# Kernel optimization log

Measured on AMD Instinct MI355X. Metric: run time of the kernel, lower is better.

Reference implementation:

```python
import jax, jax.numpy as jnp
import numpy as np

N_ELEC, N_NUC, D, F, E = 1024, 256, 64, 64, 131072
HH, HG = 128, 128
# labels: en (elec->nuc), ne (nuc->elec), same (elec->elec), anti (elec->elec)
SRC_N = [N_ELEC, N_NUC, N_ELEC, N_ELEC]
TGT_N = [N_NUC, N_ELEC, N_ELEC, N_ELEC]


def setup_inputs() -> dict:
    key = jax.random.key(0)
    ks = jax.random.split(key, 16)
    s_elec = jax.random.normal(ks[0], (N_ELEC, D), jnp.float32)
    v_elec = jax.random.normal(ks[1], (N_ELEC, D, 3), jnp.float32)
    s_nuc = jax.random.normal(ks[2], (N_NUC, D), jnp.float32)
    v_nuc = jax.random.normal(ks[3], (N_NUC, D, 3), jnp.float32)
    senders = jnp.stack([jax.random.randint(jax.random.fold_in(ks[4], i), (E,), 0, SRC_N[i]) for i in range(4)]).astype(jnp.int32)
    receivers = jnp.stack([jax.random.randint(jax.random.fold_in(ks[5], i), (E,), 0, TGT_N[i]) for i in range(4)]).astype(jnp.int32)
    dist = jax.random.uniform(ks[6], (4, E, F), jnp.float32)
    dirs = jax.random.normal(ks[7], (4, E, 3), jnp.float32)
    dirs = dirs / jnp.linalg.norm(dirs, axis=-1, keepdims=True)  # unit directions
    def w_init(k, shape):
        return jax.random.normal(k, shape, jnp.float32) / jnp.sqrt(jnp.float32(shape[-2]))
    return {
        's_elec': s_elec, 'v_elec': v_elec, 's_nuc': s_nuc, 'v_nuc': v_nuc,
        'dist': dist, 'dirs': dirs,
        'W_w': w_init(ks[8], (4, F, 3 * D)),
        'W_h1': w_init(ks[9], (4, D, HH)), 'W_h2': w_init(ks[10], (4, HH, 3 * D)),
        'W_g1': w_init(ks[11], (4, 2 * D, HG)), 'W_g2': w_init(ks[12], (4, HG, 3 * D)),
        'W_V': jnp.broadcast_to(jnp.eye(D, dtype=jnp.float32), (4, D, D)),
        'W_U': jnp.broadcast_to(jnp.eye(D, dtype=jnp.float32), (4, D, D)),
        'senders': senders, 'receivers': receivers,
    }


def _painn_layer(s_elec, v_elec, s_nuc, v_nuc, dist, dirs, W_w, W_h1, W_h2, W_g1, W_g2, W_V, W_U, senders, receivers):
    src_s = [s_elec, s_nuc, s_elec, s_elec]
    src_v = [v_elec, v_nuc, v_elec, v_elec]
    ds_e = jnp.zeros_like(s_elec); dv_e = jnp.zeros_like(v_elec)
    ds_n = jnp.zeros_like(s_nuc); dv_n = jnp.zeros_like(v_nuc)
    for i in range(4):
        n_tgt = TGT_N[i]
        # edge MLPs: w (1-layer, last linear) and h (2-layer silu, last linear), bias-free
        we = dist[i] @ W_w[i]                                   # [E, 3D]
        h_all = jax.nn.silu(src_s[i] @ W_h1[i]) @ W_h2[i]        # [n_src, 3D]
        hx = h_all[senders[i]]                                   # gather per edge
        phi_s, phi_vv, phi_vs = jnp.split(we * hx, 3, axis=-1)   # each [E, D]
        z_s = jax.ops.segment_sum(phi_s, receivers[i], n_tgt)    # [n_tgt, D]
        vv = phi_vv[..., None] * src_v[i][senders[i]]            # [E, D, 3]
        vs = phi_vs[..., None] * dirs[i][:, None, :]             # [E, D, 3]
        z_v = jax.ops.segment_sum(vv + vs, receivers[i], n_tgt)  # [n_tgt, D, 3]
        Vv = jnp.einsum('ndi,df->nfi', z_v, W_V[i])
        Uv = jnp.einsum('ndi,df->nfi', z_v, W_U[i])
        g_in = jnp.concatenate([z_s, (Vv ** 2).sum(axis=-1)], axis=-1)  # [n_tgt, 2D]
        gs = jax.nn.silu(g_in @ W_g1[i]) @ W_g2[i]               # [n_tgt, 3D]
        a_ss, a_vv, a_sv = jnp.split(gs, 3, axis=-1)
        upd_v = Uv * a_vv[..., None]
        upd_s = a_sv * jnp.einsum('nfi,nfi->nf', Uv, Vv) + a_ss
        if i == 0:  # 'en' -> nuclei
            ds_n = ds_n + upd_s; dv_n = dv_n + upd_v
        else:       # 'ne','same','anti' -> electrons
            ds_e = ds_e + upd_s; dv_e = dv_e + upd_v
    s_e = s_elec + ds_e
    v_e = v_elec + dv_e
    return jnp.concatenate([s_e, v_e.reshape(N_ELEC, -1)], axis=-1)


def reference(s_elec, v_elec, s_nuc, v_nuc, dist, dirs, W_w, W_h1, W_h2, W_g1, W_g2, W_V, W_U, senders, receivers):
    return _painn_layer(s_elec, v_elec, s_nuc, v_nuc, dist, dirs, W_w, W_h1, W_h2, W_g1, W_g2, W_V, W_U, senders, receivers)
```

## Files before the change

kernel.cpp:

```cpp
#include <hip/hip_runtime.h>
#include <stdint.h>

#define E_EDGES 131072
#define NELEC 1024
#define NNUC 256
#define MAXCHUNK 256
#define NBLK 16

typedef unsigned short ushort_t;
typedef __attribute__((ext_vector_type(8))) short short8;
typedef __attribute__((ext_vector_type(4))) short short4_t;
typedef __attribute__((ext_vector_type(4))) float float4_t;
typedef __attribute__((ext_vector_type(4))) int int4_t;
typedef __attribute__((ext_vector_type(2))) unsigned int uint2_t;

__device__ inline float silu_f(float x){ return x / (1.0f + expf(-x)); }

__device__ inline short f2bf_rne(float x){
    union { float f; uint32_t u; } a; a.f = x;
    return (short)((a.u + 0x7fffu + ((a.u >> 16) & 1u)) >> 16);
}
__device__ inline float bf2f(short h){
    union { uint32_t u; float f; } a; a.u = ((uint32_t)(uint16_t)h) << 16;
    return a.f;
}
__device__ inline ushort_t bfu(float x){ return (ushort_t)f2bf_rne(x); }
__device__ inline float asf_lo(uint32_t u){ union { uint32_t u; float f; } a; a.u = u << 16; return a.f; }
__device__ inline float asf_hi(uint32_t u){ union { uint32_t u; float f; } a; a.u = u & 0xFFFF0000u; return a.f; }

__global__ __launch_bounds__(256) void prep_kernel(
    const float* __restrict__ s_elec, const float* __restrict__ v_elec,
    const float* __restrict__ s_nuc,  const float* __restrict__ v_nuc,
    const float* __restrict__ W_h1, const float* __restrict__ W_h2,
    const float* __restrict__ W_w,
    const int* __restrict__ receivers,
    ushort_t* __restrict__ tabA, ushort_t* __restrict__ tabB,
    short* __restrict__ fragH, short* __restrict__ fragL,
    int* __restrict__ bh, float* __restrict__ out)
{
    int b = blockIdx.x, tid = threadIdx.x;
    __shared__ float sls[8][64];
    __shared__ float hidls[128][8];
    __shared__ int hist[1024];

    if (b < 288){
        int t, node0;
        if (b < 32){ t = 0; node0 = b*8; }
        else if (b < 160){ t = 1; node0 = (b-32)*8; }
        else { t = 2; node0 = (b-160)*8; }
        int tp = t + 1;
        const float* src = (t == 0) ? s_nuc : s_elec;
        const float* vsrc = (t == 0) ? v_nuc : v_elec;
        long baseA = (t == 0) ? 0 : (t == 1 ? 32768 : 163840);
        long baseB = (t == 0) ? 0 : (t == 1 ? 65536 : 327680);
        for (int i = tid; i < 512; i += 256){ int n = i >> 6, f = i & 63; sls[n][f] = src[(node0+n)*64 + f]; }
        __syncthreads();
        {
            int j = tid & 127, nh = tid >> 7;
            const float* w1 = W_h1 + (long)tp*64*128;
            float a0=0,a1=0,a2=0,a3=0;
            #pragma unroll 8
            for (int f = 0; f < 64; f++){
                float w = w1[f*128 + j];
                a0 += sls[nh*4+0][f]*w; a1 += sls[nh*4+1][f]*w;
                a2 += sls[nh*4+2][f]*w; a3 += sls[nh*4+3][f]*w;
            }
            float4_t hv = { silu_f(a0), silu_f(a1), silu_f(a2), silu_f(a3) };
            *(float4_t*)&hidls[j][nh*4] = hv;
        }
        __syncthreads();
        if (tid < 192){
            const float* w2 = W_h2 + (long)tp*128*192;
            float acc[8] = {0,0,0,0,0,0,0,0};
            #pragma unroll 4
            for (int h = 0; h < 128; h++){
                float w = w2[h*192 + tid];
                float4_t ha = *(float4_t*)&hidls[h][0];
                float4_t hb = *(float4_t*)&hidls[h][4];
                acc[0]+=ha[0]*w; acc[1]+=ha[1]*w; acc[2]+=ha[2]*w; acc[3]+=ha[3]*w;
                acc[4]+=hb[0]*w; acc[5]+=hb[1]*w; acc[6]+=hb[2]*w; acc[7]+=hb[3]*w;
            }
            int p = tid >> 6, d2 = tid & 63;
            if (p == 0){
                #pragma unroll
                for (int n = 0; n < 8; n++)
                    tabA[baseA + (long)((node0+n)*64 + d2)*2 + 0] = bfu(acc[n]);
            } else if (p == 2){
                #pragma unroll
                for (int n = 0; n < 8; n++)
                    tabA[baseA + (long)((node0+n)*64 + d2)*2 + 1] = bfu(acc[n]);
            } else {
                #pragma unroll
                for (int n = 0; n < 8; n++){
                    const float* vp = vsrc + (long)(node0+n)*192 + d2*3;
                    long o = baseB + (long)((node0+n)*64 + d2)*4;
                    tabB[o+0] = bfu(acc[n]*vp[0]);
                    tabB[o+1] = bfu(acc[n]*vp[1]);
                    tabB[o+2] = bfu(acc[n]*vp[2]);
                }
            }
        }
    } else if (b < 291){
        int t = b - 288, tp = t + 1;
        const float* W = W_w + (long)tp*64*192;
        for (int idx = tid; idx < 12288; idx += 256){
            int j    = idx & 7;
            int lane = (idx >> 3) & 63;
            int ks   = (idx >> 9) & 1;
            int nt   = idx >> 10;
            int k = ks*32 + ((lane >> 4) & 3)*8 + j;
            int n = nt*16 + (lane & 15);
            float v = W[k*192 + n];
            short hi = f2bf_rne(v);
            short lo = f2bf_rne(v - bf2f(hi));
            fragH[t*12288 + idx] = hi;
            fragL[t*12288 + idx] = lo;
        }
    } else if (b < 547){
        int i = (b - 291)*256 + tid;
        int n = i >> 6, c4 = i & 63;
        float4_t v;
        if (c4 < 16) v = *(const float4_t*)(s_elec + n*64 + c4*4);
        else         v = *(const float4_t*)(v_elec + n*192 + (c4-16)*4);
        *(float4_t*)(out + n*256 + c4*4) = v;
    } else {
        int hb = b - 547, t = hb >> 4, blk = hb & 15;
        for (int i = tid; i < 1024; i += 256) hist[i] = 0;
        __syncthreads();
        long base = (long)(t+1)*E_EDGES + blk*8192;
        #pragma unroll 4
        for (int it = 0; it < 32; it++){
            int r = receivers[base + it*256 + tid];
            atomicAdd(&hist[r], 1);
        }
        __syncthreads();
        for (int bin = tid; bin < 1024; bin += 256)
            bh[(t*1024 + bin)*NBLK + blk] = hist[bin];
    }
}

__global__ __launch_bounds__(1024) void scan_kernel(int* __restrict__ bh,
                                                    int* __restrict__ offs,
                                                    int* __restrict__ counts){
    __shared__ int buf[1024];
    int tid = threadIdx.x;
    int base = tid*48;
    int vals[48];
    const int4_t* p = (const int4_t*)(bh + base);
    int s = 0;
    #pragma unroll
    for (int j = 0; j < 12; j++){
        int4_t x = p[j];
        vals[j*4+0]=x[0]; vals[j*4+1]=x[1]; vals[j*4+2]=x[2]; vals[j*4+3]=x[3];
        s += x[0]+x[1]+x[2]+x[3];
    }
    buf[tid] = s;
    __syncthreads();
    int x = s;
    for (int off = 1; off < 1024; off <<= 1){
        int y = (tid >= off) ? buf[tid - off] : 0;
        __syncthreads();
        x += y; buf[tid] = x;
        __syncthreads();
    }
    int run = x - s;
    #pragma unroll
    for (int k = 0; k < 3; k++){
        int tb = tid*3 + k;
        offs[tb] = run;
        int c = 0;
        #pragma unroll
        for (int j = 0; j < 16; j++){
            int v = vals[k*16 + j];
            bh[base + k*16 + j] = run;
            run += v; c += v;
        }
        counts[tb] = c;
    }
}

__global__ __launch_bounds__(256) void scatter_kernel(const int* __restrict__ receivers,
                                                      const int* __restrict__ senders,
                                                      const int* __restrict__ bh,
                                                      int* __restrict__ sorted){
    int hb = blockIdx.x, t = hb >> 4, blk = hb & 15;
    int tid = threadIdx.x;
    __shared__ int cur[1024];
    for (int bin = tid; bin < 1024; bin += 256) cur[bin] = bh[(t*1024 + bin)*NBLK + blk];
    __syncthreads();
    long base = (long)(t+1)*E_EDGES + blk*8192;
    #pragma unroll 2
    for (int it = 0; it < 32; it++){
        int e = blk*8192 + it*256 + tid;
        int r = receivers[base + it*256 + tid];
        int snd = senders[base + it*256 + tid];
        int pos = atomicAdd(&cur[r], 1);
        sorted[pos] = e | (snd << 17);
    }
}

__global__ __launch_bounds__(256) void main_kernel(
    const float* __restrict__ dist, const float* __restrict__ dirs,
    const float* __restrict__ W_V, const float* __restrict__ W_U,
    const float* __restrict__ W_g1, const float* __restrict__ W_g2,
    const ushort_t* __restrict__ tabA, const ushort_t* __restrict__ tabB,
    const short* __restrict__ fragH, const short* __restrict__ fragL,
    const int* __restrict__ counts, const int* __restrict__ offs, const int* __restrict__ sorted,
    float* __restrict__ out)
{
    int b = blockIdx.x;
    int t = b >> 10, node = b & 1023, tp = t + 1;
    const ushort_t* ta = tabA + ((t == 0) ? 0 : (t == 1 ? 32768 : 163840));
    const ushort_t* tb = tabB + ((t == 0) ? 0 : (t == 1 ? 65536 : 327680));
    const float* dbase = dist + (long)tp*E_EDGES*64;
    const float* dirbase = dirs + (long)tp*E_EDGES*3;

    int tid = threadIdx.x;
    int w = tid >> 6, l = tid & 63;
    int q = l >> 4, c16 = l & 15;
    int d = w*16 + c16;

    __shared__ short AH[2][2][64][8];
    __shared__ short AL[2][2][64][8];
    __shared__ float dls[2][16][3];
    __shared__ int eid[MAXCHUNK];
    __shared__ int sid[MAXCHUNK];
    __shared__ float zs[64];
    __shared__ float zv[64][3];
    __shared__ float VvL[192], UvL[192];
    __shared__ float gin[128], hidl[128], aL[192], vdotL[64];

    short8 bhf[3][2], blf[3][2];
    #pragma unroll
    for (int ni = 0; ni < 3; ni++){
        int nt = w + ni*4;
        #pragma unroll
        for (int ks = 0; ks < 2; ks++){
            long base = (long)t*12288 + ((nt*2 + ks)*64 + l)*8;
            bhf[ni][ks] = *(const short8*)(fragH + base);
            blf[ni][ks] = *(const short8*)(fragL + base);
        }
    }

    float acc_s = 0.f, acc_v0 = 0.f, acc_v1 = 0.f, acc_v2 = 0.f;

    int deg   = counts[t*1024 + node];
    int start = offs[t*1024 + node];

    int m = tid >> 4, seg = tid & 15;
    int ks_w = seg >> 3, quad_w = (seg >> 1) & 3, j0_w = (seg & 1)*4;
    int lane2 = m | (quad_w << 4);
    int mm = tid / 3, ii = tid - mm*3;

    const float4_t z4 = {0.f,0.f,0.f,0.f};

    for (int cbase = 0; cbase < deg; cbase += MAXCHUNK){
        int chunk = deg - cbase; if (chunk > MAXCHUNK) chunk = MAXCHUNK;
        __syncthreads();
        {
            int v = 0;
            if (tid < chunk) v = sorted[(long)start + cbase + tid];
            eid[tid] = v & 131071;
            sid[tid] = ((unsigned)v) >> 17;
        }
        __syncthreads();

        int ngroups = (chunk + 15) >> 4;
        float4_t dv = z4;
        if (m < chunk) dv = *(const float4_t*)(dbase + (long)eid[m]*64 + seg*4);
        float dirv = 0.f;
        if (tid < 48 && mm < chunk) dirv = dirbase[(long)eid[mm]*3 + ii];
        uint32_t gA[4]; uint2_t gB[4];
        #pragma unroll
        for (int r = 0; r < 4; r++){
            int s = sid[q*4 + r];
            gA[r] = *(const uint32_t*)(ta + (long)(s*64 + d)*2);
            gB[r] = *(const uint2_t*)(tb + (long)(s*64 + d)*4);
        }

        for (int g = 0; g < ngroups; g++){
            int buf = g & 1;
            {
                short4_t h4, l4;
                #pragma unroll
                for (int jj = 0; jj < 4; jj++){
                    short hi = f2bf_rne(dv[jj]);
                    h4[jj] = hi;
                    l4[jj] = f2bf_rne(dv[jj] - bf2f(hi));
                }
                *(short4_t*)&AH[buf][ks_w][lane2][j0_w] = h4;
                *(short4_t*)&AL[buf][ks_w][lane2][j0_w] = l4;
                if (tid < 48) dls[buf][mm][ii] = dirv;
            }
            float4_t dvn = z4; float dirn = 0.f;
            uint32_t gAn[4] = {0,0,0,0}; uint2_t gBn[4] = {{0,0},{0,0},{0,0},{0,0}};
            if (g + 1 < ngroups){
                int li = (g+1)*16 + m;
                if (li < chunk) dvn = *(const float4_t*)(dbase + (long)eid[li]*64 + seg*4);
                int li2 = (g+1)*16 + mm;
                if (tid < 48 && li2 < chunk) dirn = dirbase[(long)eid[li2]*3 + ii];
                #pragma unroll
                for (int r = 0; r < 4; r++){
                    int s = sid[(g+1)*16 + q*4 + r];
                    gAn[r] = *(const uint32_t*)(ta + (long)(s*64 + d)*2);
                    gBn[r] = *(const uint2_t*)(tb + (long)(s*64 + d)*4);
                }
            }
            __syncthreads();

            short8 ah0 = *(short8*)&AH[buf][0][l][0];
            short8 ah1 = *(short8*)&AH[buf][1][l][0];
            short8 al0 = *(short8*)&AL[buf][0][l][0];
            short8 al1 = *(short8*)&AL[buf][1][l][0];
            float4_t C[3];
            #pragma unroll
            for (int ni = 0; ni < 3; ni++){
                float4_t acc = z4;
                acc = __builtin_amdgcn_mfma_f32_16x16x32_bf16(ah0, bhf[ni][0], acc, 0, 0, 0);
                acc = __builtin_amdgcn_mfma_f32_16x16x32_bf16(ah1, bhf[ni][1], acc, 0, 0, 0);
                acc = __builtin_amdgcn_mfma_f32_16x16x32_bf16(ah0, blf[ni][0], acc, 0, 0, 0);
                acc = __builtin_amdgcn_mfma_f32_16x16x32_bf16(ah1, blf[ni][1], acc, 0, 0, 0);
                acc = __builtin_amdgcn_mfma_f32_16x16x32_bf16(al0, bhf[ni][0], acc, 0, 0, 0);
                acc = __builtin_amdgcn_mfma_f32_16x16x32_bf16(al1, bhf[ni][1], acc, 0, 0, 0);
                C[ni] = acc;
            }

            #pragma unroll
            for (int r = 0; r < 4; r++){
                int mr = q*4 + r;
                float hs  = asf_lo(gA[r]);
                float hvs = asf_hi(gA[r]);
                float hv0 = asf_lo(gB[r][0]);
                float hv1 = asf_hi(gB[r][0]);
                float hv2 = asf_lo(gB[r][1]);
                acc_s += C[0][r] * hs;
                float pvs = C[2][r] * hvs;
                acc_v0 += C[1][r]*hv0 + pvs * dls[buf][mr][0];
                acc_v1 += C[1][r]*hv1 + pvs * dls[buf][mr][1];
                acc_v2 += C[1][r]*hv2 + pvs * dls[buf][mr][2];
            }
            dv = dvn; dirv = dirn;
            #pragma unroll
            for (int r = 0; r < 4; r++){ gA[r] = gAn[r]; gB[r] = gBn[r]; }
        }
    }

    acc_s  += __shfl_xor(acc_s, 16);  acc_s  += __shfl_xor(acc_s, 32);
    acc_v0 += __shfl_xor(acc_v0, 16); acc_v0 += __shfl_xor(acc_v0, 32);
    acc_v1 += __shfl_xor(acc_v1, 16); acc_v1 += __shfl_xor(acc_v1, 32);
    acc_v2 += __shfl_xor(acc_v2, 16); acc_v2 += __shfl_xor(acc_v2, 32);
    __syncthreads();
    if (l < 16){
        zs[d] = acc_s;
        zv[d][0] = acc_v0; zv[d][1] = acc_v1; zv[d][2] = acc_v2;
    }
    __syncthreads();

    if (tid < 192){
        int i = tid >> 6, f = tid & 63;
        const float* wv = W_V + (long)tp*64*64;
        const float* wu = W_U + (long)tp*64*64;
        float av = 0.f, au = 0.f;
        #pragma unroll 8
        for (int dd = 0; dd < 64; dd++){
            float z = zv[dd][i];
            av += z * wv[dd*64 + f];
            au += z * wu[dd*64 + f];
        }
        VvL[f*3 + i] = av;
        UvL[f*3 + i] = au;
    }
    __syncthreads();
    if (tid < 64){
        int f = tid;
        float v0 = VvL[f*3], v1 = VvL[f*3+1], v2 = VvL[f*3+2];
        float u0 = UvL[f*3], u1 = UvL[f*3+1], u2 = UvL[f*3+2];
        gin[f] = zs[f];
        gin[64 + f] = v0*v0 + v1*v1 + v2*v2;
        vdotL[f] = u0*v0 + u1*v1 + u2*v2;
    }
    __syncthreads();
    if (tid < 128){
        const float* w1 = W_g1 + (long)tp*128*128;
        float acc = 0.f;
        #pragma unroll 8
        for (int c = 0; c < 128; c++) acc += gin[c] * w1[c*128 + tid];
        hidl[tid] = silu_f(acc);
    }
    __syncthreads();
    if (tid < 192){
        const float* w2 = W_g2 + (long)tp*128*192;
        float acc = 0.f;
        #pragma unroll 8
        for (int h = 0; h < 128; h++) acc += hidl[h] * w2[h*192 + tid];
        aL[tid] = acc;
    }
    __syncthreads();
    if (tid < 64){
        int f = tid;
        float upd = aL[128 + f] * vdotL[f] + aL[f];
        atomicAdd(&out[node*256 + f], upd);
    }
    if (tid < 192){
        int i = tid >> 6, f = tid & 63;
        float updv = UvL[f*3 + i] * aL[64 + f];
        atomicAdd(&out[node*256 + 64 + f*3 + i], updv);
    }
}

extern "C" void kernel_launch(void* const* d_in, const int* in_sizes, int n_in,
                              void* d_out, int out_size, void* d_ws, size_t ws_size,
                              hipStream_t stream){
    const float* s_elec  = (const float*)d_in[0];
    const float* v_elec  = (const float*)d_in[1];
    const float* s_nuc   = (const float*)d_in[2];
    const float* v_nuc   = (const float*)d_in[3];
    const float* dist    = (const float*)d_in[4];
    const float* dirs    = (const float*)d_in[5];
    const float* W_w     = (const float*)d_in[6];
    const float* W_h1    = (const float*)d_in[7];
    const float* W_h2    = (const float*)d_in[8];
    const float* W_g1    = (const float*)d_in[9];
    const float* W_g2    = (const float*)d_in[10];
    const float* W_V     = (const float*)d_in[11];
    const float* W_U     = (const float*)d_in[12];
    const int* senders   = (const int*)d_in[13];
    const int* receivers = (const int*)d_in[14];
    float* out = (float*)d_out;
    char* ws = (char*)d_ws;

    ushort_t* tabA  = (ushort_t*)(ws + 0);
    ushort_t* tabB  = (ushort_t*)(ws + 589824);
    short* fragH  = (short*)(ws + 1769472);
    short* fragL  = (short*)(ws + 1843200);
    int*   bh     = (int*)  (ws + 1916928);
    int*   offs   = (int*)  (ws + 2113536);
    int*   counts = (int*)  (ws + 2125824);
    int*   sorted = (int*)  (ws + 2138112);
    if (ws_size < 3710976) return;

    prep_kernel<<<dim3(595), dim3(256), 0, stream>>>(
        s_elec, v_elec, s_nuc, v_nuc, W_h1, W_h2, W_w, receivers,
        tabA, tabB, fragH, fragL, bh, out);
    scan_kernel<<<dim3(1), dim3(1024), 0, stream>>>(bh, offs, counts);
    scatter_kernel<<<dim3(48), dim3(256), 0, stream>>>(receivers, senders, bh, sorted);
    main_kernel<<<dim3(3072), dim3(256), 0, stream>>>(
        dist, dirs, W_V, W_U, W_g1, W_g2,
        tabA, tabB, fragH, fragL, counts, offs, sorted, out);
}
```

Baseline: 363.3 us.

## Pre-gather edge distance and direction rows into receiver-sorted order before main kernel

Adds a reorder kernel that copies each edge's dist row and dirs vector into a workspace buffer in receiver-sorted order. The main kernel, templated on this path, then streams contiguous rows instead of gathering scattered 256-byte rows through edge ids. The goal is to turn the main kernel's random gathers into coalesced sequential reads. The cost is an extra pass that reads and writes roughly 100 MB of workspace. The new path runs only when the workspace is large enough; otherwise the old gather path is used.

```diff
diff --git a/kernel.cpp b/kernel.cpp
--- a/kernel.cpp
+++ b/kernel.cpp
@@ -199,8 +199,38 @@
     }
 }
 
+__global__ __launch_bounds__(256) void reorder_kernel(const float* __restrict__ dist,
+                                                      const float* __restrict__ dirs,
+                                                      const int* __restrict__ sorted,
+                                                      float* __restrict__ wsdist,
+                                                      float* __restrict__ wsdirs){
+    int tid = threadIdx.x;
+    long base = (long)blockIdx.x * 64;
+    #pragma unroll
+    for (int it = 0; it < 4; it++){
+        int idx = it*256 + tid;
+        int row = idx >> 4, chunk = idx & 15;
+        long i = base + row;
+        int v = sorted[i];
+        int t = (int)(i >> 17);
+        int e = v & 131071;
+        float4_t x = *(const float4_t*)(dist + ((long)(t+1)*E_EDGES + e)*64 + chunk*4);
+        *(float4_t*)(wsdist + i*64 + chunk*4) = x;
+    }
+    for (int j = tid; j < 192; j += 256){
+        int row = j / 3, c = j - row*3;
+        long i = base + row;
+        int v = sorted[i];
+        int t = (int)(i >> 17);
+        int e = v & 131071;
+        wsdirs[i*3 + c] = dirs[((long)(t+1)*E_EDGES + e)*3 + c];
+    }
+}
+
+template<bool RO>
 __global__ __launch_bounds__(256) void main_kernel(
     const float* __restrict__ dist, const float* __restrict__ dirs,
+    const float* __restrict__ wsdist, const float* __restrict__ wsdirs,
     const float* __restrict__ W_V, const float* __restrict__ W_U,
     const float* __restrict__ W_g1, const float* __restrict__ W_g2,
     const ushort_t* __restrict__ tabA, const ushort_t* __restrict__ tabB,
@@ -267,9 +297,15 @@
 
         int ngroups = (chunk + 15) >> 4;
         float4_t dv = z4;
-        if (m < chunk) dv = *(const float4_t*)(dbase + (long)eid[m]*64 + seg*4);
+        if (m < chunk){
+            if (RO) dv = *(const float4_t*)(wsdist + (long)(start + cbase + m)*64 + seg*4);
+            else    dv = *(const float4_t*)(dbase + (long)eid[m]*64 + seg*4);
+        }
         float dirv = 0.f;
-        if (tid < 48 && mm < chunk) dirv = dirbase[(long)eid[mm]*3 + ii];
+        if (tid < 48 && mm < chunk){
+            if (RO) dirv = wsdirs[(long)(start + cbase + mm)*3 + ii];
+            else    dirv = dirbase[(long)eid[mm]*3 + ii];
+        }
         uint32_t gA[4]; uint2_t gB[4];
         #pragma unroll
         for (int r = 0; r < 4; r++){
@@ -296,9 +332,15 @@
             uint32_t gAn[4] = {0,0,0,0}; uint2_t gBn[4] = {{0,0},{0,0},{0,0},{0,0}};
             if (g + 1 < ngroups){
                 int li = (g+1)*16 + m;
-                if (li < chunk) dvn = *(const float4_t*)(dbase + (long)eid[li]*64 + seg*4);
+                if (li < chunk){
+                    if (RO) dvn = *(const float4_t*)(wsdist + (long)(start + cbase + li)*64 + seg*4);
+                    else    dvn = *(const float4_t*)(dbase + (long)eid[li]*64 + seg*4);
+                }
                 int li2 = (g+1)*16 + mm;
-                if (tid < 48 && li2 < chunk) dirn = dirbase[(long)eid[li2]*3 + ii];
+                if (tid < 48 && li2 < chunk){
+                    if (RO) dirn = wsdirs[(long)(start + cbase + li2)*3 + ii];
+                    else    dirn = dirbase[(long)eid[li2]*3 + ii];
+                }
                 #pragma unroll
                 for (int r = 0; r < 4; r++){
                     int s = sid[(g+1)*16 + q*4 + r];
@@ -437,14 +479,24 @@
     int*   offs   = (int*)  (ws + 2113536);
     int*   counts = (int*)  (ws + 2125824);
     int*   sorted = (int*)  (ws + 2138112);
+    float* wsdist = (float*)(ws + 3710976);
+    float* wsdirs = (float*)(ws + 104374272);
     if (ws_size < 3710976) return;
+    bool big = (ws_size >= 109092864);
 
     prep_kernel<<<dim3(595), dim3(256), 0, stream>>>(
         s_elec, v_elec, s_nuc, v_nuc, W_h1, W_h2, W_w, receivers,
         tabA, tabB, fragH, fragL, bh, out);
     scan_kernel<<<dim3(1), dim3(1024), 0, stream>>>(bh, offs, counts);
     scatter_kernel<<<dim3(48), dim3(256), 0, stream>>>(receivers, senders, bh, sorted);
-    main_kernel<<<dim3(3072), dim3(256), 0, stream>>>(
-        dist, dirs, W_V, W_U, W_g1, W_g2,
-        tabA, tabB, fragH, fragL, counts, offs, sorted, out);
-}
+    if (big){
+        reorder_kernel<<<dim3(6144), dim3(256), 0, stream>>>(dist, dirs, sorted, wsdist, wsdirs);
+        main_kernel<true><<<dim3(3072), dim3(256), 0, stream>>>(
+            dist, dirs, wsdist, wsdirs, W_V, W_U, W_g1, W_g2,
+            tabA, tabB, fragH, fragL, counts, offs, sorted, out);
+    } else {
+        main_kernel<false><<<dim3(3072), dim3(256), 0, stream>>>(
+            dist, dirs, wsdist, wsdirs, W_V, W_U, W_g1, W_g2,
+            tabA, tabB, fragH, fragL, counts, offs, sorted, out);
+    }
+}
```

Result: slower. 399.6 us (+10.0%).
